# Kernel optimization log

Measured on AMD Instinct MI355X. Metric: run time of the kernel, lower is better.

## Reference

```python
import jax, jax.numpy as jnp
import numpy as np

N = 2048      # spatial nodes
K = 4         # blanket size (timesteps)
C = 128       # channels
H = 4         # heads
D = C // H    # head dim
MOD = 256     # mod_features
CTX = 7       # context_features (3+4)
B = 1
TN = N * K


def _make_edges():
    """Faithful numpy port of create_spatio_temporal_edges."""
    rng = np.random.default_rng(0)
    loops = np.stack([np.arange(N), np.arange(N)], axis=1)
    rnd = rng.integers(0, N, size=(N * 15, 2))
    self_edges = np.concatenate([loops, rnd])          # (32768, 2), every node has an edge
    cross_edges = rng.integers(0, N, size=(N * 8, 2))  # (16384, 2)
    spatial = (np.arange(K)[:, None, None] * N + self_edges[None]).reshape(-1, 2)
    temporal = (np.arange(K)[:, None, None] * N + cross_edges[None]).reshape(-1, 2)
    tq, tk = temporal[:, 0], temporal[:, 1]
    E = cross_edges.shape[0]
    parts = [spatial] + [np.stack([tq, np.roll(tk, -(k + 1) * E)], axis=-1) for k in range(K - 1)]
    return np.concatenate(parts).astype(np.int32)   # (327680, 2)


def setup_inputs() -> dict:
    key = jax.random.key(0)
    ks = jax.random.split(key, 16)
    def g(i, shape, scale=0.02):
        return jax.random.normal(ks[i], shape, dtype=jnp.float32) * scale
    return {
        "x": jax.random.normal(ks[0], (B, TN, C), dtype=jnp.float32),
        "time_encoding": jax.random.normal(ks[1], (B, MOD), dtype=jnp.float32),
        "context_encoding": jax.random.normal(ks[2], (B, K, N, CTX), dtype=jnp.float32),
        "edge_index": jnp.asarray(_make_edges()),
        "mod_w1": g(3, (MOD, MOD)), "mod_b1": jnp.zeros((MOD,), jnp.float32),
        "mod_w2": g(4, (3 * C, MOD), 0.0002), "mod_b2": jnp.zeros((3 * C,), jnp.float32),  # last linear scaled by 0.01
        "siren_w0": g(5, (C, CTX), 0.5), "siren_b0": jnp.zeros((C,), jnp.float32),
        "siren_w1": g(6, (C, C)), "siren_b1": jnp.zeros((C,), jnp.float32),
        "wq": g(7, (C, C)), "bq": jnp.zeros((C,), jnp.float32),
        "wk": g(8, (C, C)), "bk": jnp.zeros((C,), jnp.float32),
        "wv": g(9, (C, C)), "bv": jnp.zeros((C,), jnp.float32),
        "wo": g(10, (C, C)), "bo": jnp.zeros((C,), jnp.float32),
        "ffn_w1": g(11, (4 * C, C)), "ffn_b1": jnp.zeros((4 * C,), jnp.float32),
        "ffn_w2": g(12, (C, 4 * C)), "ffn_b2": jnp.zeros((C,), jnp.float32),
    }


def _ln(z, eps=1e-5):
    m = jnp.mean(z, axis=-1, keepdims=True)
    v = jnp.var(z, axis=-1, keepdims=True)
    return (z - m) * jax.lax.rsqrt(v + eps)


def reference(x, time_encoding, context_encoding, edge_index,
              mod_w1, mod_b1, mod_w2, mod_b2,
              siren_w0, siren_b0, siren_w1, siren_b1,
              wq, bq, wk, bk, wv, bv, wo, bo,
              ffn_w1, ffn_b1, ffn_w2, ffn_b2):
    Bx, TNx, Cx = x.shape
    Dh = Cx // H
    # AdaLN modulation: Linear -> SiLU -> Linear -> split into (a, b, c), each (B,1,C)
    t = jax.nn.silu(time_encoding @ mod_w1.T + mod_b1)
    mod = (t @ mod_w2.T + mod_b2).reshape(Bx, 3, Cx)
    a, b, c = mod[:, 0][:, None, :], mod[:, 1][:, None, :], mod[:, 2][:, None, :]
    # SIREN context embedding (1 sin layer + output linear)
    hctx = jnp.sin(context_encoding @ siren_w0.T + siren_b0)
    ctx = (hctx @ siren_w1.T + siren_b1).reshape(Bx, TNx, Cx)
    y = (a + 1.0) * _ln(x + ctx) + b
    # Graph attention over edge list (qk_norm = per-head LayerNorm, no affine)
    q = _ln((y @ wq.T + bq).reshape(Bx, TNx, H, Dh))
    k = _ln((y @ wk.T + bk).reshape(Bx, TNx, H, Dh))
    v = (y @ wv.T + bv).reshape(Bx, TNx, H, Dh)
    src, dst = edge_index[:, 0], edge_index[:, 1]  # query node, key node
    qT = jnp.transpose(q, (1, 0, 2, 3))  # (TN,B,H,D): segment axis first
    kT = jnp.transpose(k, (1, 0, 2, 3))
    vT = jnp.transpose(v, (1, 0, 2, 3))
    qe, ke, ve = qT[src], kT[dst], vT[dst]             # (E,B,H,D)
    s = jnp.einsum('ebhd,ebhd->ebh', qe, ke) / jnp.sqrt(jnp.float32(Dh))
    m = jax.ops.segment_max(s, src, num_segments=TNx)  # (TN,B,H)
    p = jnp.exp(s - m[src])
    denom = jax.ops.segment_sum(p, src, num_segments=TNx)
    agg = jax.ops.segment_sum(p[..., None] * ve, src, num_segments=TNx)  # (TN,B,H,D)
    attn = agg / jnp.maximum(denom, 1e-9)[..., None]
    attn = jnp.transpose(attn, (1, 0, 2, 3)).reshape(Bx, TNx, Cx) @ wo.T + bo
    y = y + attn
    # FFN (no inner residual, matches original)
    y = jax.nn.silu(y @ ffn_w1.T + ffn_b1) @ ffn_w2.T + ffn_b2
    # rsqrt-scaled residual combine
    return (x + c * y) * jax.lax.rsqrt(1.0 + c * c)
```

## Files before the change

kernel.cpp:

```cpp
#include <hip/hip_runtime.h>
#include <math.h>

#define TNODES 8192
#define CC 128
#define RT 32
#define DEGCAP 128

typedef __attribute__((ext_vector_type(8))) short bf8;
typedef __attribute__((ext_vector_type(4))) float fx4;

__device__ __forceinline__ ushort f2b(float f){
  union { float f; uint u; } a; a.f = f;
  uint u = a.u;
  uint r = (u + 0x7fffu + ((u >> 16) & 1u)) >> 16;
  return (ushort)r;
}
__device__ __forceinline__ float b2f(ushort s){
  union { uint u; float f; } a; a.u = ((uint)s) << 16;
  return a.f;
}
__device__ __forceinline__ float2 bpair(uint u){
  union { uint u; float f; } lo, hi;
  lo.u = u << 16; hi.u = u & 0xffff0000u;
  float2 r; r.x = lo.f; r.y = hi.f; return r;
}
#define SWZ(row, col) ((col) ^ (((row) & 7) << 3))

__global__ __launch_bounds__(256) void s1_setup(
    const float* __restrict__ sw1, const float* __restrict__ wq, const float* __restrict__ wk,
    const float* __restrict__ wv, const float* __restrict__ wo, const float* __restrict__ fw1,
    const float* __restrict__ fw2, ushort* __restrict__ dst,
    int* __restrict__ cnt,
    const float* __restrict__ te, const float* __restrict__ mw1, const float* __restrict__ mb1,
    float* __restrict__ tbuf)
{
  const int b = blockIdx.x, tid = threadIdx.x;
  if (b < 208){
    int i = (b * 256 + tid) * 4;
    const float* src; int off;
    if      (i <  16384){ src = sw1; off = i; }
    else if (i <  32768){ src = wq;  off = i - 16384; }
    else if (i <  49152){ src = wk;  off = i - 32768; }
    else if (i <  65536){ src = wv;  off = i - 49152; }
    else if (i <  81920){ src = wo;  off = i - 65536; }
    else if (i < 147456){ src = fw1; off = i - 81920; }
    else                { src = fw2; off = i - 147456; }
    float4 v = *(const float4*)&src[off];
    ushort4 o; o.x = f2b(v.x); o.y = f2b(v.y); o.z = f2b(v.z); o.w = f2b(v.w);
    *(ushort4*)&dst[i] = o;
  } else if (b < 240){
    cnt[(b - 208) * 256 + tid] = 0;
  } else {
    const int og = tid >> 4, th = tid & 15;
    const int o = (b - 240) * 16 + og;
    float acc = 0.f;
    #pragma unroll
    for (int u = 0; u < 4; ++u){
      float4 w  = *(const float4*)&mw1[o*256 + th*16 + u*4];
      float4 t4 = *(const float4*)&te[th*16 + u*4];
      acc += w.x*t4.x + w.y*t4.y + w.z*t4.z + w.w*t4.w;
    }
    #pragma unroll
    for (int m = 1; m < 16; m <<= 1) acc += __shfl_xor(acc, m);
    if (th == 0){
      float z = acc + mb1[o];
      tbuf[o] = z / (1.f + __expf(-z));
    }
  }
}

__global__ __launch_bounds__(512) void k2_ctx_y_qkv(
    const float* __restrict__ x, const float* __restrict__ ce,
    const float* __restrict__ sw0, const float* __restrict__ sb0,
    const ushort* __restrict__ sw1b, const float* __restrict__ sb1,
    const ushort* __restrict__ wqb, const float* __restrict__ bq,
    const ushort* __restrict__ wkb, const float* __restrict__ bk,
    const ushort* __restrict__ wvb, const float* __restrict__ bv,
    const float* __restrict__ tbuf, const float* __restrict__ mw2, const float* __restrict__ mb2,
    ushort* __restrict__ Ybf, ushort* __restrict__ Qb, ushort* __restrict__ Kb, ushort* __restrict__ Vb,
    const int* __restrict__ ei, int E, int* __restrict__ cnt, int* __restrict__ adj)
{
  __shared__ float  ceL[RT][8];
  __shared__ float  tbL[256];
  __shared__ float  modL[256];
  __shared__ ushort hxb[RT*CC];
  __shared__ float  yL[RT][132];
  __shared__ ushort yb[RT*CC];
  const int tid  = threadIdx.x;

  if (blockIdx.x >= TNODES/RT){
    const int b = blockIdx.x - TNODES/RT;
    int e0 = (b * 512 + tid) * 2;
    if (e0 + 1 < E){
      int4 p = *(const int4*)&ei[2*e0];
      int s;
      s = atomicAdd(&cnt[p.x], 1); adj[p.x*DEGCAP + (s & (DEGCAP-1))] = p.y;
      s = atomicAdd(&cnt[p.z], 1); adj[p.z*DEGCAP + (s & (DEGCAP-1))] = p.w;
    } else if (e0 < E){
      int sr = ei[2*e0], ds = ei[2*e0+1];
      int s = atomicAdd(&cnt[sr], 1);
      adj[sr*DEGCAP + (s & (DEGCAP-1))] = ds;
    }
    return;
  }

  const int lane = tid & 63, wave = tid >> 6;
  const int l15 = lane & 15, lg = lane >> 4;
  const int hw  = wave & 3;
  const int rtb = (wave >> 2) * 16;
  const int row0 = blockIdx.x * RT;

  if (tid < RT*7){ int r = tid/7, i = tid - r*7; ceL[r][i] = ce[(row0+r)*7 + i]; }
  if (tid < 256) tbL[tid] = tbuf[tid];
  __syncthreads();

  #pragma unroll
  for (int u = 0; u < 8; ++u){
    int idx = tid + u*512;
    int r = idx >> 7, j = idx & 127;
    float a = sb0[j];
    #pragma unroll
    for (int i = 0; i < 7; ++i) a += sw0[j*7+i]*ceL[r][i];
    hxb[r*CC + SWZ(r, j)] = f2b(__sinf(a));
  }

  {
    const int g = tid >> 4, th = tid & 15;
    #pragma unroll
    for (int it = 0; it < 8; ++it){
      int o = g*8 + it;
      float acc = 0.f;
      #pragma unroll
      for (int u = 0; u < 4; ++u){
        float4 wv = *(const float4*)&mw2[o*256 + th*16 + u*4];
        float4 t4 = *(const float4*)&tbL[th*16 + u*4];
        acc += wv.x*t4.x + wv.y*t4.y + wv.z*t4.z + wv.w*t4.w;
      }
      #pragma unroll
      for (int m = 1; m < 16; m <<= 1) acc += __shfl_xor(acc, m);
      if (th == 0) modL[o] = acc + mb2[o];
    }
  }
  __syncthreads();

  const int colb = hw*32;
  {
    bf8 aH[4], bB[8];
    #pragma unroll
    for (int ks = 0; ks < 4; ++ks)
      aH[ks] = *(const bf8*)&hxb[(rtb+l15)*CC + SWZ(rtb+l15, ks*32 + lg*8)];
    #pragma unroll
    for (int ks = 0; ks < 4; ++ks)
      #pragma unroll
      for (int n = 0; n < 2; ++n)
        bB[ks*2+n] = *(const bf8*)&sw1b[(colb + n*16 + l15)*CC + ks*32 + lg*8];
    fx4 acc[2]; acc[0] = 0.f; acc[1] = 0.f;
    #pragma unroll
    for (int ks = 0; ks < 4; ++ks){
      acc[0] = __builtin_amdgcn_mfma_f32_16x16x32_bf16(aH[ks], bB[ks*2+0], acc[0], 0, 0, 0);
      acc[1] = __builtin_amdgcn_mfma_f32_16x16x32_bf16(aH[ks], bB[ks*2+1], acc[1], 0, 0, 0);
    }
    #pragma unroll
    for (int n = 0; n < 2; ++n)
      #pragma unroll
      for (int q = 0; q < 4; ++q){
        int r = rtb + lg*4 + q, c = colb + n*16 + l15;
        yL[r][c] = x[(row0+r)*CC + c] + acc[n][q] + sb1[c];
      }
  }
  __syncthreads();

  {
    int r = tid >> 4, s16 = tid & 15;
    float4 za = *(const float4*)&yL[r][s16*8];
    float4 zb = *(const float4*)&yL[r][s16*8 + 4];
    float sum = za.x+za.y+za.z+za.w + zb.x+zb.y+zb.z+zb.w;
    float ssq = za.x*za.x+za.y*za.y+za.z*za.z+za.w*za.w
              + zb.x*zb.x+zb.y*zb.y+zb.z*zb.z+zb.w*zb.w;
    #pragma unroll
    for (int m = 1; m < 16; m <<= 1){ sum += __shfl_xor(sum, m); ssq += __shfl_xor(ssq, m); }
    float mean = sum * (1.f/128.f);
    float var  = ssq * (1.f/128.f) - mean*mean;
    float inv  = rsqrtf(var + 1e-5f);
    float zv[8] = {za.x,za.y,za.z,za.w,zb.x,zb.y,zb.z,zb.w};
    bf8 pk;
    #pragma unroll
    for (int u = 0; u < 8; ++u){
      int jj = s16*8 + u;
      float z = (zv[u] - mean) * inv;
      pk[u] = (short)f2b((1.f + modL[jj]) * z + modL[128+jj]);
    }
    *(bf8*)&yb[r*CC + SWZ(r, s16*8)] = pk;
  }
  __syncthreads();

  {
    int rr = tid >> 4, b8 = tid & 15;
    bf8 v = *(const bf8*)&yb[rr*CC + SWZ(rr, b8*8)];
    *(bf8*)&Ybf[(row0+rr)*CC + b8*8] = v;
  }

  bf8 af[4];
  #pragma unroll
  for (int ks = 0; ks < 4; ++ks)
    af[ks] = *(const bf8*)&yb[(rtb+l15)*CC + SWZ(rtb+l15, ks*32 + lg*8)];

  const ushort* Wb[3] = {wqb, wkb, wvb};
  const float*  Bs[3] = {bq, bk, bv};
  ushort*       Ob[3] = {Qb, Kb, Vb};
  const int cb = hw*32;
  #pragma unroll
  for (int m = 0; m < 3; ++m){
    bf8 bB[8];
    #pragma unroll
    for (int ks = 0; ks < 4; ++ks)
      #pragma unroll
      for (int n = 0; n < 2; ++n)
        bB[ks*2+n] = *(const bf8*)&Wb[m][(cb + n*16 + l15)*CC + ks*32 + lg*8];
    fx4 acc[2]; acc[0] = 0.f; acc[1] = 0.f;
    #pragma unroll
    for (int ks = 0; ks < 4; ++ks){
      acc[0] = __builtin_amdgcn_mfma_f32_16x16x32_bf16(af[ks], bB[ks*2+0], acc[0], 0, 0, 0);
      acc[1] = __builtin_amdgcn_mfma_f32_16x16x32_bf16(af[ks], bB[ks*2+1], acc[1], 0, 0, 0);
    }
    float vals[2][4];
    #pragma unroll
    for (int n = 0; n < 2; ++n)
      #pragma unroll
      for (int q = 0; q < 4; ++q)
        vals[n][q] = acc[n][q] + Bs[m][cb + n*16 + l15];
    if (m < 2){
      #pragma unroll
      for (int q = 0; q < 4; ++q){
        float s  = vals[0][q] + vals[1][q];
        float ss = vals[0][q]*vals[0][q] + vals[1][q]*vals[1][q];
        #pragma unroll
        for (int mm = 1; mm < 16; mm <<= 1){ s += __shfl_xor(s, mm); ss += __shfl_xor(ss, mm); }
        float mean = s * (1.f/32.f);
        float var  = ss * (1.f/32.f) - mean*mean;
        float inv  = rsqrtf(var + 1e-5f);
        vals[0][q] = (vals[0][q] - mean) * inv;
        vals[1][q] = (vals[1][q] - mean) * inv;
      }
    }
    #pragma unroll
    for (int n = 0; n < 2; ++n)
      #pragma unroll
      for (int q = 0; q < 4; ++q){
        int r = rtb + lg*4 + q, c = cb + n*16 + l15;
        Ob[m][(row0+r)*CC + c] = f2b(vals[n][q]);
      }
  }
}

__global__ __launch_bounds__(512) void k45_attn_ffn(
    const float* __restrict__ x, const ushort* __restrict__ Ybf,
    const ushort* __restrict__ Qb, const ushort* __restrict__ Kb, const ushort* __restrict__ Vb,
    const int* __restrict__ cnt, const int* __restrict__ adj,
    const ushort* __restrict__ wob, const float* __restrict__ bo,
    const ushort* __restrict__ fw1b, const float* __restrict__ fb1,
    const ushort* __restrict__ fw2b, const float* __restrict__ fb2,
    const float* __restrict__ tbuf, const float* __restrict__ mw2, const float* __restrict__ mb2,
    float* __restrict__ out)
{
  __shared__ float  tbL[256];
  __shared__ float  cL[128];
  __shared__ ushort aLb[RT*CC];
  __shared__ ushort yyb[RT*CC];
  __shared__ ushort h1b[RT*512];
  const int tid  = threadIdx.x;
  const int lane = tid & 63, w = tid >> 6;
  const int l15 = lane & 15, lg = lane >> 4;
  const int row0 = blockIdx.x * RT;

  if (tid < 256) tbL[tid] = tbuf[tid];
  __syncthreads();

  {
    const int g = tid >> 4, th = tid & 15;
    #pragma unroll
    for (int it = 0; it < 4; ++it){
      int o = g*4 + it;
      float acc = 0.f;
      #pragma unroll
      for (int u = 0; u < 4; ++u){
        float4 wv = *(const float4*)&mw2[(256+o)*256 + th*16 + u*4];
        float4 t4 = *(const float4*)&tbL[th*16 + u*4];
        acc += wv.x*t4.x + wv.y*t4.y + wv.z*t4.z + wv.w*t4.w;
      }
      #pragma unroll
      for (int m = 1; m < 16; m <<= 1) acc += __shfl_xor(acc, m);
      if (th == 0) cL[o] = acc + mb2[256+o];
    }
  }

  {
    const int quarter = lane >> 4, ql = lane & 15;
    const int src = row0 + w*4 + quarter;

    uint4 qr = *(const uint4*)&Qb[src*CC + 8*ql];
    float2 qa = bpair(qr.x), qb = bpair(qr.y), qc = bpair(qr.z), qd = bpair(qr.w);
    const float sc = 0.17677669529663687f;
    qa.x*=sc; qa.y*=sc; qb.x*=sc; qb.y*=sc; qc.x*=sc; qc.y*=sc; qd.x*=sc; qd.y*=sc;

    float a0=0.f,a1=0.f,a2=0.f,a3=0.f,a4=0.f,a5=0.f,a6=0.f,a7=0.f, dh=0.f;
    const int deg = min(cnt[src], DEGCAP);
    const int* ab = adj + src*DEGCAP;
    int dmax = deg;
    dmax = max(dmax, __shfl_xor(dmax, 16));
    dmax = max(dmax, __shfl_xor(dmax, 32));

    for (int e = 0; e < dmax; e += 4){
      int4 dd = *(const int4*)&ab[e];
      int d0 = (e   < deg) ? dd.x : 0;
      int d1 = (e+1 < deg) ? dd.y : 0;
      int d2 = (e+2 < deg) ? dd.z : 0;
      int d3 = (e+3 < deg) ? dd.w : 0;
      uint4 k0 = *(const uint4*)&Kb[d0*CC + 8*ql];
      uint4 k1 = *(const uint4*)&Kb[d1*CC + 8*ql];
      uint4 k2 = *(const uint4*)&Kb[d2*CC + 8*ql];
      uint4 k3 = *(const uint4*)&Kb[d3*CC + 8*ql];
      uint4 v0 = *(const uint4*)&Vb[d0*CC + 8*ql];
      uint4 v1 = *(const uint4*)&Vb[d1*CC + 8*ql];
      uint4 v2 = *(const uint4*)&Vb[d2*CC + 8*ql];
      uint4 v3 = *(const uint4*)&Vb[d3*CC + 8*ql];
      float2 x0, x1, x2, x3;
      x0 = bpair(k0.x); x1 = bpair(k0.y); x2 = bpair(k0.z); x3 = bpair(k0.w);
      float p0 = qa.x*x0.x+qa.y*x0.y + qb.x*x1.x+qb.y*x1.y + qc.x*x2.x+qc.y*x2.y + qd.x*x3.x+qd.y*x3.y;
      x0 = bpair(k1.x); x1 = bpair(k1.y); x2 = bpair(k1.z); x3 = bpair(k1.w);
      float p1 = qa.x*x0.x+qa.y*x0.y + qb.x*x1.x+qb.y*x1.y + qc.x*x2.x+qc.y*x2.y + qd.x*x3.x+qd.y*x3.y;
      x0 = bpair(k2.x); x1 = bpair(k2.y); x2 = bpair(k2.z); x3 = bpair(k2.w);
      float p2 = qa.x*x0.x+qa.y*x0.y + qb.x*x1.x+qb.y*x1.y + qc.x*x2.x+qc.y*x2.y + qd.x*x3.x+qd.y*x3.y;
      x0 = bpair(k3.x); x1 = bpair(k3.y); x2 = bpair(k3.z); x3 = bpair(k3.w);
      float p3 = qa.x*x0.x+qa.y*x0.y + qb.x*x1.x+qb.y*x1.y + qc.x*x2.x+qc.y*x2.y + qd.x*x3.x+qd.y*x3.y;
      p0 += __shfl_xor(p0, 1); p1 += __shfl_xor(p1, 1); p2 += __shfl_xor(p2, 1); p3 += __shfl_xor(p3, 1);
      p0 += __shfl_xor(p0, 2); p1 += __shfl_xor(p1, 2); p2 += __shfl_xor(p2, 2); p3 += __shfl_xor(p3, 2);
      p0 = (e   < deg) ? __expf(p0) : 0.f;
      p1 = (e+1 < deg) ? __expf(p1) : 0.f;
      p2 = (e+2 < deg) ? __expf(p2) : 0.f;
      p3 = (e+3 < deg) ? __expf(p3) : 0.f;
      x0 = bpair(v0.x); x1 = bpair(v0.y); x2 = bpair(v0.z); x3 = bpair(v0.w);
      a0 += p0*x0.x; a1 += p0*x0.y; a2 += p0*x1.x; a3 += p0*x1.y;
      a4 += p0*x2.x; a5 += p0*x2.y; a6 += p0*x3.x; a7 += p0*x3.y;
      x0 = bpair(v1.x); x1 = bpair(v1.y); x2 = bpair(v1.z); x3 = bpair(v1.w);
      a0 += p1*x0.x; a1 += p1*x0.y; a2 += p1*x1.x; a3 += p1*x1.y;
      a4 += p1*x2.x; a5 += p1*x2.y; a6 += p1*x3.x; a7 += p1*x3.y;
      x0 = bpair(v2.x); x1 = bpair(v2.y); x2 = bpair(v2.z); x3 = bpair(v2.w);
      a0 += p2*x0.x; a1 += p2*x0.y; a2 += p2*x1.x; a3 += p2*x1.y;
      a4 += p2*x2.x; a5 += p2*x2.y; a6 += p2*x3.x; a7 += p2*x3.y;
      x0 = bpair(v3.x); x1 = bpair(v3.y); x2 = bpair(v3.z); x3 = bpair(v3.w);
      a0 += p3*x0.x; a1 += p3*x0.y; a2 += p3*x1.x; a3 += p3*x1.y;
      a4 += p3*x2.x; a5 += p3*x2.y; a6 += p3*x3.x; a7 += p3*x3.y;
      dh += p0 + p1 + p2 + p3;
    }
    float invd = 1.f / fmaxf(dh, 1e-9f);
    uint4 o4;
    o4.x = (uint)f2b(a0*invd) | ((uint)f2b(a1*invd) << 16);
    o4.y = (uint)f2b(a2*invd) | ((uint)f2b(a3*invd) << 16);
    o4.z = (uint)f2b(a4*invd) | ((uint)f2b(a5*invd) << 16);
    o4.w = (uint)f2b(a6*invd) | ((uint)f2b(a7*invd) << 16);
    int r = w*4 + quarter;
    *(uint4*)&aLb[r*CC + SWZ(r, 8*ql)] = o4;
  }
  __syncthreads();

  {
    const int cw = w*16;
    bf8 aA[2][4], bB[4];
    #pragma unroll
    for (int rt = 0; rt < 2; ++rt)
      #pragma unroll
      for (int ks = 0; ks < 4; ++ks)
        aA[rt][ks] = *(const bf8*)&aLb[(rt*16+l15)*CC + SWZ(rt*16+l15, ks*32 + lg*8)];
    #pragma unroll
    for (int ks = 0; ks < 4; ++ks)
      bB[ks] = *(const bf8*)&wob[(cw + l15)*CC + ks*32 + lg*8];
    fx4 acc[2]; acc[0] = 0.f; acc[1] = 0.f;
    #pragma unroll
    for (int ks = 0; ks < 4; ++ks){
      acc[0] = __builtin_amdgcn_mfma_f32_16x16x32_bf16(aA[0][ks], bB[ks], acc[0], 0, 0, 0);
      acc[1] = __builtin_amdgcn_mfma_f32_16x16x32_bf16(aA[1][ks], bB[ks], acc[1], 0, 0, 0);
    }
    #pragma unroll
    for (int rt = 0; rt < 2; ++rt)
      #pragma unroll
      for (int q = 0; q < 4; ++q){
        int r = rt*16 + lg*4 + q, c = cw + l15;
        float yy = b2f(Ybf[(row0+r)*CC + c]) + acc[rt][q] + bo[c];
        yyb[r*CC + SWZ(r, c)] = f2b(yy);
      }
  }
  __syncthreads();

  {
    const int cb1 = w*64;
    bf8 aY[2][4];
    #pragma unroll
    for (int rt = 0; rt < 2; ++rt)
      #pragma unroll
      for (int ks = 0; ks < 4; ++ks)
        aY[rt][ks] = *(const bf8*)&yyb[(rt*16+l15)*CC + SWZ(rt*16+l15, ks*32 + lg*8)];
    fx4 h[2][4];
    #pragma unroll
    for (int rt = 0; rt < 2; ++rt)
      #pragma unroll
      for (int n = 0; n < 4; ++n) h[rt][n] = 0.f;
    #pragma unroll
    for (int kp = 0; kp < 2; ++kp){
      bf8 bB[8];
      #pragma unroll
      for (int kk = 0; kk < 2; ++kk)
        #pragma unroll
        for (int n = 0; n < 4; ++n)
          bB[kk*4+n] = *(const bf8*)&fw1b[(cb1 + n*16 + l15)*CC + (kp*2+kk)*32 + lg*8];
      #pragma unroll
      for (int kk = 0; kk < 2; ++kk)
        #pragma unroll
        for (int n = 0; n < 4; ++n){
          h[0][n] = __builtin_amdgcn_mfma_f32_16x16x32_bf16(aY[0][kp*2+kk], bB[kk*4+n], h[0][n], 0, 0, 0);
          h[1][n] = __builtin_amdgcn_mfma_f32_16x16x32_bf16(aY[1][kp*2+kk], bB[kk*4+n], h[1][n], 0, 0, 0);
        }
    }
    #pragma unroll
    for (int rt = 0; rt < 2; ++rt)
      #pragma unroll
      for (int n = 0; n < 4; ++n)
        #pragma unroll
        for (int q = 0; q < 4; ++q){
          int r = rt*16 + lg*4 + q, c = cb1 + n*16 + l15;
          float z = h[rt][n][q] + fb1[c];
          float sl = z / (1.f + __expf(-z));
          h1b[r*512 + SWZ(r, c)] = f2b(sl);
        }
  }
  __syncthreads();

  {
    const int cw = w*16;
    fx4 acc[2]; acc[0] = 0.f; acc[1] = 0.f;
    #pragma unroll
    for (int g4 = 0; g4 < 4; ++g4){
      bf8 aH[2][4], bB[4];
      #pragma unroll
      for (int rt = 0; rt < 2; ++rt)
        #pragma unroll
        for (int kk = 0; kk < 4; ++kk)
          aH[rt][kk] = *(const bf8*)&h1b[(rt*16+l15)*512 + SWZ(rt*16+l15, (g4*4+kk)*32 + lg*8)];
      #pragma unroll
      for (int kk = 0; kk < 4; ++kk)
        bB[kk] = *(const bf8*)&fw2b[(cw + l15)*512 + (g4*4+kk)*32 + lg*8];
      #pragma unroll
      for (int kk = 0; kk < 4; ++kk){
        acc[0] = __builtin_amdgcn_mfma_f32_16x16x32_bf16(aH[0][kk], bB[kk], acc[0], 0, 0, 0);
        acc[1] = __builtin_amdgcn_mfma_f32_16x16x32_bf16(aH[1][kk], bB[kk], acc[1], 0, 0, 0);
      }
    }
    #pragma unroll
    for (int rt = 0; rt < 2; ++rt)
      #pragma unroll
      for (int q = 0; q < 4; ++q){
        int r = rt*16 + lg*4 + q, c = cw + l15;
        int g = row0 + r;
        float cj = cL[c];
        float y2 = acc[rt][q] + fb2[c];
        out[g*CC + c] = (x[g*CC + c] + cj*y2) * rsqrtf(1.f + cj*cj);
      }
  }
}

extern "C" void kernel_launch(void* const* d_in, const int* in_sizes, int n_in,
                              void* d_out, int out_size, void* d_ws, size_t ws_size,
                              hipStream_t stream)
{
  const float* x   = (const float*)d_in[0];
  const float* te  = (const float*)d_in[1];
  const float* ce  = (const float*)d_in[2];
  const int*   ei  = (const int*)  d_in[3];
  const float* mw1 = (const float*)d_in[4];
  const float* mb1 = (const float*)d_in[5];
  const float* mw2 = (const float*)d_in[6];
  const float* mb2 = (const float*)d_in[7];
  const float* sw0 = (const float*)d_in[8];
  const float* sb0 = (const float*)d_in[9];
  const float* sw1 = (const float*)d_in[10];
  const float* sb1 = (const float*)d_in[11];
  const float* wq  = (const float*)d_in[12];
  const float* bq  = (const float*)d_in[13];
  const float* wk  = (const float*)d_in[14];
  const float* bk  = (const float*)d_in[15];
  const float* wv  = (const float*)d_in[16];
  const float* bv  = (const float*)d_in[17];
  const float* wo  = (const float*)d_in[18];
  const float* bo  = (const float*)d_in[19];
  const float* fw1 = (const float*)d_in[20];
  const float* fb1 = (const float*)d_in[21];
  const float* fw2 = (const float*)d_in[22];
  const float* fb2 = (const float*)d_in[23];
  float* out = (float*)d_out;
  const int E = in_sizes[3] / 2;

  float* ws   = (float*)d_ws;
  float* tbuf = ws;
  ushort* WB  = (ushort*)(ws + 1024);
  ushort* sw1b = WB;
  ushort* wqb  = WB + 16384;
  ushort* wkb  = WB + 32768;
  ushort* wvb  = WB + 49152;
  ushort* wob  = WB + 65536;
  ushort* fw1b = WB + 81920;
  ushort* fw2b = WB + 147456;
  ushort* Ybf = WB + 212992;
  ushort* Qb  = Ybf + TNODES*CC;
  ushort* Kb  = Qb  + TNODES*CC;
  ushort* Vb  = Kb  + TNODES*CC;
  int* cnt    = (int*)(Vb + TNODES*CC);
  int* adj    = cnt + TNODES;

  const int nSB = (E + 1023) / 1024;

  s1_setup<<<256, 256, 0, stream>>>(sw1, wq, wk, wv, wo, fw1, fw2, WB, cnt, te, mw1, mb1, tbuf);
  k2_ctx_y_qkv<<<TNODES/RT + nSB, 512, 0, stream>>>(x, ce, sw0, sb0, sw1b, sb1,
                                              wqb, bq, wkb, bk, wvb, bv,
                                              tbuf, mw2, mb2, Ybf, Qb, Kb, Vb,
                                              ei, E, cnt, adj);
  k45_attn_ffn<<<TNODES/RT, 512, 0, stream>>>(x, Ybf, Qb, Kb, Vb, cnt, adj,
                                              wob, bo, fw1b, fb1, fw2b, fb2,
                                              tbuf, mw2, mb2, out);
}
```

Measured before the change: 73.42 us.

## Halve attention/FFN row tile, spread each node over 32 lanes, prefetch gathers

The fused attention+FFN kernel now handles 16 rows per block instead of 32, doubling the grid, and asks for 4 blocks per CU through launch bounds. In the edge-gather loop each source node is served by 32 lanes loading 4 bf16 values each instead of 16 lanes loading 8, so fewer rows sit idle waiting on the slowest neighbour. The K/V gathers for the next group of 4 edges are software-prefetched into registers. The aim is more latency hiding for the irregular gather, at the cost of an extra shuffle step, more register pressure and re-reading the weights from twice as many blocks in the MFMA stages.

```diff
diff --git a/kernel.cpp b/kernel.cpp
--- a/kernel.cpp
+++ b/kernel.cpp
@@ -3,7 +3,8 @@
 
 #define TNODES 8192
 #define CC 128
-#define RT 32
+#define RT2 32
+#define RT5 16
 #define DEGCAP 128
 
 typedef __attribute__((ext_vector_type(8))) short bf8;
@@ -80,16 +81,16 @@
     ushort* __restrict__ Ybf, ushort* __restrict__ Qb, ushort* __restrict__ Kb, ushort* __restrict__ Vb,
     const int* __restrict__ ei, int E, int* __restrict__ cnt, int* __restrict__ adj)
 {
-  __shared__ float  ceL[RT][8];
+  __shared__ float  ceL[RT2][8];
   __shared__ float  tbL[256];
   __shared__ float  modL[256];
-  __shared__ ushort hxb[RT*CC];
-  __shared__ float  yL[RT][132];
-  __shared__ ushort yb[RT*CC];
+  __shared__ ushort hxb[RT2*CC];
+  __shared__ float  yL[RT2][132];
+  __shared__ ushort yb[RT2*CC];
   const int tid  = threadIdx.x;
 
-  if (blockIdx.x >= TNODES/RT){
-    const int b = blockIdx.x - TNODES/RT;
+  if (blockIdx.x >= TNODES/RT2){
+    const int b = blockIdx.x - TNODES/RT2;
     int e0 = (b * 512 + tid) * 2;
     if (e0 + 1 < E){
       int4 p = *(const int4*)&ei[2*e0];
@@ -108,9 +109,9 @@
   const int l15 = lane & 15, lg = lane >> 4;
   const int hw  = wave & 3;
   const int rtb = (wave >> 2) * 16;
-  const int row0 = blockIdx.x * RT;
-
-  if (tid < RT*7){ int r = tid/7, i = tid - r*7; ceL[r][i] = ce[(row0+r)*7 + i]; }
+  const int row0 = blockIdx.x * RT2;
+
+  if (tid < RT2*7){ int r = tid/7, i = tid - r*7; ceL[r][i] = ce[(row0+r)*7 + i]; }
   if (tid < 256) tbL[tid] = tbuf[tid];
   __syncthreads();
 
@@ -253,7 +254,7 @@
   }
 }
 
-__global__ __launch_bounds__(512) void k45_attn_ffn(
+__global__ __launch_bounds__(512, 4) void k45_attn_ffn(
     const float* __restrict__ x, const ushort* __restrict__ Ybf,
     const ushort* __restrict__ Qb, const ushort* __restrict__ Kb, const ushort* __restrict__ Vb,
     const int* __restrict__ cnt, const int* __restrict__ adj,
@@ -265,13 +266,13 @@
 {
   __shared__ float  tbL[256];
   __shared__ float  cL[128];
-  __shared__ ushort aLb[RT*CC];
-  __shared__ ushort yyb[RT*CC];
-  __shared__ ushort h1b[RT*512];
+  __shared__ ushort aLb[RT5*CC];
+  __shared__ ushort yyb[RT5*CC];
+  __shared__ ushort h1b[RT5*512];
   const int tid  = threadIdx.x;
   const int lane = tid & 63, w = tid >> 6;
   const int l15 = lane & 15, lg = lane >> 4;
-  const int row0 = blockIdx.x * RT;
+  const int row0 = blockIdx.x * RT5;
 
   if (tid < 256) tbL[tid] = tbuf[tid];
   __syncthreads();
@@ -295,116 +296,122 @@
   }
 
   {
-    const int quarter = lane >> 4, ql = lane & 15;
-    const int src = row0 + w*4 + quarter;
-
-    uint4 qr = *(const uint4*)&Qb[src*CC + 8*ql];
-    float2 qa = bpair(qr.x), qb = bpair(qr.y), qc = bpair(qr.z), qd = bpair(qr.w);
+    const int half = lane >> 5, hl = lane & 31;
+    const int src = row0 + w*2 + half;
+
+    uint2 qraw = *(const uint2*)&Qb[src*CC + 4*hl];
+    float2 q0 = bpair(qraw.x), q1 = bpair(qraw.y);
     const float sc = 0.17677669529663687f;
-    qa.x*=sc; qa.y*=sc; qb.x*=sc; qb.y*=sc; qc.x*=sc; qc.y*=sc; qd.x*=sc; qd.y*=sc;
-
-    float a0=0.f,a1=0.f,a2=0.f,a3=0.f,a4=0.f,a5=0.f,a6=0.f,a7=0.f, dh=0.f;
+    q0.x*=sc; q0.y*=sc; q1.x*=sc; q1.y*=sc;
+
+    float a0=0.f, a1=0.f, a2=0.f, a3=0.f, dh=0.f;
     const int deg = min(cnt[src], DEGCAP);
     const int* ab = adj + src*DEGCAP;
-    int dmax = deg;
-    dmax = max(dmax, __shfl_xor(dmax, 16));
-    dmax = max(dmax, __shfl_xor(dmax, 32));
-
-    for (int e = 0; e < dmax; e += 4){
-      int4 dd = *(const int4*)&ab[e];
-      int d0 = (e   < deg) ? dd.x : 0;
-      int d1 = (e+1 < deg) ? dd.y : 0;
-      int d2 = (e+2 < deg) ? dd.z : 0;
-      int d3 = (e+3 < deg) ? dd.w : 0;
-      uint4 k0 = *(const uint4*)&Kb[d0*CC + 8*ql];
-      uint4 k1 = *(const uint4*)&Kb[d1*CC + 8*ql];
-      uint4 k2 = *(const uint4*)&Kb[d2*CC + 8*ql];
-      uint4 k3 = *(const uint4*)&Kb[d3*CC + 8*ql];
-      uint4 v0 = *(const uint4*)&Vb[d0*CC + 8*ql];
-      uint4 v1 = *(const uint4*)&Vb[d1*CC + 8*ql];
-      uint4 v2 = *(const uint4*)&Vb[d2*CC + 8*ql];
-      uint4 v3 = *(const uint4*)&Vb[d3*CC + 8*ql];
-      float2 x0, x1, x2, x3;
-      x0 = bpair(k0.x); x1 = bpair(k0.y); x2 = bpair(k0.z); x3 = bpair(k0.w);
-      float p0 = qa.x*x0.x+qa.y*x0.y + qb.x*x1.x+qb.y*x1.y + qc.x*x2.x+qc.y*x2.y + qd.x*x3.x+qd.y*x3.y;
-      x0 = bpair(k1.x); x1 = bpair(k1.y); x2 = bpair(k1.z); x3 = bpair(k1.w);
-      float p1 = qa.x*x0.x+qa.y*x0.y + qb.x*x1.x+qb.y*x1.y + qc.x*x2.x+qc.y*x2.y + qd.x*x3.x+qd.y*x3.y;
-      x0 = bpair(k2.x); x1 = bpair(k2.y); x2 = bpair(k2.z); x3 = bpair(k2.w);
-      float p2 = qa.x*x0.x+qa.y*x0.y + qb.x*x1.x+qb.y*x1.y + qc.x*x2.x+qc.y*x2.y + qd.x*x3.x+qd.y*x3.y;
-      x0 = bpair(k3.x); x1 = bpair(k3.y); x2 = bpair(k3.z); x3 = bpair(k3.w);
-      float p3 = qa.x*x0.x+qa.y*x0.y + qb.x*x1.x+qb.y*x1.y + qc.x*x2.x+qc.y*x2.y + qd.x*x3.x+qd.y*x3.y;
+    int dmax = max(deg, __shfl_xor(deg, 32));
+    const int niter = (dmax + 3) >> 2;
+
+    uint2 k0,k1,k2,k3,v0,v1,v2,v3;
+    {
+      int4 dd = *(const int4*)&ab[0];
+      int d0 = dd.x;
+      int d1 = (1 < deg) ? dd.y : 0;
+      int d2 = (2 < deg) ? dd.z : 0;
+      int d3 = (3 < deg) ? dd.w : 0;
+      k0 = *(const uint2*)&Kb[d0*CC + 4*hl];
+      k1 = *(const uint2*)&Kb[d1*CC + 4*hl];
+      k2 = *(const uint2*)&Kb[d2*CC + 4*hl];
+      k3 = *(const uint2*)&Kb[d3*CC + 4*hl];
+      v0 = *(const uint2*)&Vb[d0*CC + 4*hl];
+      v1 = *(const uint2*)&Vb[d1*CC + 4*hl];
+      v2 = *(const uint2*)&Vb[d2*CC + 4*hl];
+      v3 = *(const uint2*)&Vb[d3*CC + 4*hl];
+    }
+
+    for (int i = 0; i < niter; ++i){
+      const int e = i*4;
+      uint2 ck0=k0, ck1=k1, ck2=k2, ck3=k3, cv0=v0, cv1=v1, cv2=v2, cv3=v3;
+      if (i + 1 < niter){
+        int en = e + 4;
+        int4 dd = *(const int4*)&ab[en];
+        int d0 = (en   < deg) ? dd.x : 0;
+        int d1 = (en+1 < deg) ? dd.y : 0;
+        int d2 = (en+2 < deg) ? dd.z : 0;
+        int d3 = (en+3 < deg) ? dd.w : 0;
+        k0 = *(const uint2*)&Kb[d0*CC + 4*hl];
+        k1 = *(const uint2*)&Kb[d1*CC + 4*hl];
+        k2 = *(const uint2*)&Kb[d2*CC + 4*hl];
+        k3 = *(const uint2*)&Kb[d3*CC + 4*hl];
+        v0 = *(const uint2*)&Vb[d0*CC + 4*hl];
+        v1 = *(const uint2*)&Vb[d1*CC + 4*hl];
+        v2 = *(const uint2*)&Vb[d2*CC + 4*hl];
+        v3 = *(const uint2*)&Vb[d3*CC + 4*hl];
+      }
+      float2 f0, f1;
+      f0 = bpair(ck0.x); f1 = bpair(ck0.y);
+      float p0 = q0.x*f0.x + q0.y*f0.y + q1.x*f1.x + q1.y*f1.y;
+      f0 = bpair(ck1.x); f1 = bpair(ck1.y);
+      float p1 = q0.x*f0.x + q0.y*f0.y + q1.x*f1.x + q1.y*f1.y;
+      f0 = bpair(ck2.x); f1 = bpair(ck2.y);
+      float p2 = q0.x*f0.x + q0.y*f0.y + q1.x*f1.x + q1.y*f1.y;
+      f0 = bpair(ck3.x); f1 = bpair(ck3.y);
+      float p3 = q0.x*f0.x + q0.y*f0.y + q1.x*f1.x + q1.y*f1.y;
       p0 += __shfl_xor(p0, 1); p1 += __shfl_xor(p1, 1); p2 += __shfl_xor(p2, 1); p3 += __shfl_xor(p3, 1);
       p0 += __shfl_xor(p0, 2); p1 += __shfl_xor(p1, 2); p2 += __shfl_xor(p2, 2); p3 += __shfl_xor(p3, 2);
+      p0 += __shfl_xor(p0, 4); p1 += __shfl_xor(p1, 4); p2 += __shfl_xor(p2, 4); p3 += __shfl_xor(p3, 4);
       p0 = (e   < deg) ? __expf(p0) : 0.f;
       p1 = (e+1 < deg) ? __expf(p1) : 0.f;
       p2 = (e+2 < deg) ? __expf(p2) : 0.f;
       p3 = (e+3 < deg) ? __expf(p3) : 0.f;
-      x0 = bpair(v0.x); x1 = bpair(v0.y); x2 = bpair(v0.z); x3 = bpair(v0.w);
-      a0 += p0*x0.x; a1 += p0*x0.y; a2 += p0*x1.x; a3 += p0*x1.y;
-      a4 += p0*x2.x; a5 += p0*x2.y; a6 += p0*x3.x; a7 += p0*x3.y;
-      x0 = bpair(v1.x); x1 = bpair(v1.y); x2 = bpair(v1.z); x3 = bpair(v1.w);
-      a0 += p1*x0.x; a1 += p1*x0.y; a2 += p1*x1.x; a3 += p1*x1.y;
-      a4 += p1*x2.x; a5 += p1*x2.y; a6 += p1*x3.x; a7 += p1*x3.y;
-      x0 = bpair(v2.x); x1 = bpair(v2.y); x2 = bpair(v2.z); x3 = bpair(v2.w);
-      a0 += p2*x0.x; a1 += p2*x0.y; a2 += p2*x1.x; a3 += p2*x1.y;
-      a4 += p2*x2.x; a5 += p2*x2.y; a6 += p2*x3.x; a7 += p2*x3.y;
-      x0 = bpair(v3.x); x1 = bpair(v3.y); x2 = bpair(v3.z); x3 = bpair(v3.w);
-      a0 += p3*x0.x; a1 += p3*x0.y; a2 += p3*x1.x; a3 += p3*x1.y;
-      a4 += p3*x2.x; a5 += p3*x2.y; a6 += p3*x3.x; a7 += p3*x3.y;
+      f0 = bpair(cv0.x); f1 = bpair(cv0.y);
+      a0 += p0*f0.x; a1 += p0*f0.y; a2 += p0*f1.x; a3 += p0*f1.y;
+      f0 = bpair(cv1.x); f1 = bpair(cv1.y);
+      a0 += p1*f0.x; a1 += p1*f0.y; a2 += p1*f1.x; a3 += p1*f1.y;
+      f0 = bpair(cv2.x); f1 = bpair(cv2.y);
+      a0 += p2*f0.x; a1 += p2*f0.y; a2 += p2*f1.x; a3 += p2*f1.y;
+      f0 = bpair(cv3.x); f1 = bpair(cv3.y);
+      a0 += p3*f0.x; a1 += p3*f0.y; a2 += p3*f1.x; a3 += p3*f1.y;
       dh += p0 + p1 + p2 + p3;
     }
     float invd = 1.f / fmaxf(dh, 1e-9f);
-    uint4 o4;
-    o4.x = (uint)f2b(a0*invd) | ((uint)f2b(a1*invd) << 16);
-    o4.y = (uint)f2b(a2*invd) | ((uint)f2b(a3*invd) << 16);
-    o4.z = (uint)f2b(a4*invd) | ((uint)f2b(a5*invd) << 16);
-    o4.w = (uint)f2b(a6*invd) | ((uint)f2b(a7*invd) << 16);
-    int r = w*4 + quarter;
-    *(uint4*)&aLb[r*CC + SWZ(r, 8*ql)] = o4;
+    uint2 o2;
+    o2.x = (uint)f2b(a0*invd) | ((uint)f2b(a1*invd) << 16);
+    o2.y = (uint)f2b(a2*invd) | ((uint)f2b(a3*invd) << 16);
+    int r = w*2 + half;
+    *(uint2*)&aLb[r*CC + SWZ(r, 4*hl)] = o2;
   }
   __syncthreads();
 
   {
     const int cw = w*16;
-    bf8 aA[2][4], bB[4];
-    #pragma unroll
-    for (int rt = 0; rt < 2; ++rt)
-      #pragma unroll
-      for (int ks = 0; ks < 4; ++ks)
-        aA[rt][ks] = *(const bf8*)&aLb[(rt*16+l15)*CC + SWZ(rt*16+l15, ks*32 + lg*8)];
+    bf8 aA[4], bB[4];
+    #pragma unroll
+    for (int ks = 0; ks < 4; ++ks)
+      aA[ks] = *(const bf8*)&aLb[l15*CC + SWZ(l15, ks*32 + lg*8)];
     #pragma unroll
     for (int ks = 0; ks < 4; ++ks)
       bB[ks] = *(const bf8*)&wob[(cw + l15)*CC + ks*32 + lg*8];
-    fx4 acc[2]; acc[0] = 0.f; acc[1] = 0.f;
-    #pragma unroll
-    for (int ks = 0; ks < 4; ++ks){
-      acc[0] = __builtin_amdgcn_mfma_f32_16x16x32_bf16(aA[0][ks], bB[ks], acc[0], 0, 0, 0);
-      acc[1] = __builtin_amdgcn_mfma_f32_16x16x32_bf16(aA[1][ks], bB[ks], acc[1], 0, 0, 0);
-    }
-    #pragma unroll
-    for (int rt = 0; rt < 2; ++rt)
-      #pragma unroll
-      for (int q = 0; q < 4; ++q){
-        int r = rt*16 + lg*4 + q, c = cw + l15;
-        float yy = b2f(Ybf[(row0+r)*CC + c]) + acc[rt][q] + bo[c];
-        yyb[r*CC + SWZ(r, c)] = f2b(yy);
-      }
+    fx4 acc; acc = 0.f;
+    #pragma unroll
+    for (int ks = 0; ks < 4; ++ks)
+      acc = __builtin_amdgcn_mfma_f32_16x16x32_bf16(aA[ks], bB[ks], acc, 0, 0, 0);
+    #pragma unroll
+    for (int q = 0; q < 4; ++q){
+      int r = lg*4 + q, c = cw + l15;
+      float yy = b2f(Ybf[(row0+r)*CC + c]) + acc[q] + bo[c];
+      yyb[r*CC + SWZ(r, c)] = f2b(yy);
+    }
   }
   __syncthreads();
 
   {
     const int cb1 = w*64;
-    bf8 aY[2][4];
-    #pragma unroll
-    for (int rt = 0; rt < 2; ++rt)
-      #pragma unroll
-      for (int ks = 0; ks < 4; ++ks)
-        aY[rt][ks] = *(const bf8*)&yyb[(rt*16+l15)*CC + SWZ(rt*16+l15, ks*32 + lg*8)];
-    fx4 h[2][4];
-    #pragma unroll
-    for (int rt = 0; rt < 2; ++rt)
-      #pragma unroll
-      for (int n = 0; n < 4; ++n) h[rt][n] = 0.f;
+    bf8 aY[4];
+    #pragma unroll
+    for (int ks = 0; ks < 4; ++ks)
+      aY[ks] = *(const bf8*)&yyb[l15*CC + SWZ(l15, ks*32 + lg*8)];
+    fx4 h[4];
+    #pragma unroll
+    for (int n = 0; n < 4; ++n) h[n] = 0.f;
     #pragma unroll
     for (int kp = 0; kp < 2; ++kp){
       bf8 bB[8];
@@ -416,55 +423,45 @@
       #pragma unroll
       for (int kk = 0; kk < 2; ++kk)
         #pragma unroll
-        for (int n = 0; n < 4; ++n){
-          h[0][n] = __builtin_amdgcn_mfma_f32_16x16x32_bf16(aY[0][kp*2+kk], bB[kk*4+n], h[0][n], 0, 0, 0);
-          h[1][n] = __builtin_amdgcn_mfma_f32_16x16x32_bf16(aY[1][kp*2+kk], bB[kk*4+n], h[1][n], 0, 0, 0);
-        }
-    }
-    #pragma unroll
-    for (int rt = 0; rt < 2; ++rt)
-      #pragma unroll
-      for (int n = 0; n < 4; ++n)
-        #pragma unroll
-        for (int q = 0; q < 4; ++q){
-          int r = rt*16 + lg*4 + q, c = cb1 + n*16 + l15;
-          float z = h[rt][n][q] + fb1[c];
-          float sl = z / (1.f + __expf(-z));
-          h1b[r*512 + SWZ(r, c)] = f2b(sl);
-        }
+        for (int n = 0; n < 4; ++n)
+          h[n] = __builtin_amdgcn_mfma_f32_16x16x32_bf16(aY[kp*2+kk], bB[kk*4+n], h[n], 0, 0, 0);
+    }
+    #pragma unroll
+    for (int n = 0; n < 4; ++n)
+      #pragma unroll
+      for (int q = 0; q < 4; ++q){
+        int r = lg*4 + q, c = cb1 + n*16 + l15;
+        float z = h[n][q] + fb1[c];
+        float sl = z / (1.f + __expf(-z));
+        h1b[r*512 + SWZ(r, c)] = f2b(sl);
+      }
   }
   __syncthreads();
 
   {
     const int cw = w*16;
-    fx4 acc[2]; acc[0] = 0.f; acc[1] = 0.f;
+    fx4 acc; acc = 0.f;
     #pragma unroll
     for (int g4 = 0; g4 < 4; ++g4){
-      bf8 aH[2][4], bB[4];
-      #pragma unroll
-      for (int rt = 0; rt < 2; ++rt)
-        #pragma unroll
-        for (int kk = 0; kk < 4; ++kk)
-          aH[rt][kk] = *(const bf8*)&h1b[(rt*16+l15)*512 + SWZ(rt*16+l15, (g4*4+kk)*32 + lg*8)];
+      bf8 aH[4], bB[4];
+      #pragma unroll
+      for (int kk = 0; kk < 4; ++kk)
+        aH[kk] = *(const bf8*)&h1b[l15*512 + SWZ(l15, (g4*4+kk)*32 + lg*8)];
       #pragma unroll
       for (int kk = 0; kk < 4; ++kk)
         bB[kk] = *(const bf8*)&fw2b[(cw + l15)*512 + (g4*4+kk)*32 + lg*8];
       #pragma unroll
-      for (int kk = 0; kk < 4; ++kk){
-        acc[0] = __builtin_amdgcn_mfma_f32_16x16x32_bf16(aH[0][kk], bB[kk], acc[0], 0, 0, 0);
-        acc[1] = __builtin_amdgcn_mfma_f32_16x16x32_bf16(aH[1][kk], bB[kk], acc[1], 0, 0, 0);
-      }
-    }
-    #pragma unroll
-    for (int rt = 0; rt < 2; ++rt)
-      #pragma unroll
-      for (int q = 0; q < 4; ++q){
-        int r = rt*16 + lg*4 + q, c = cw + l15;
-        int g = row0 + r;
-        float cj = cL[c];
-        float y2 = acc[rt][q] + fb2[c];
-        out[g*CC + c] = (x[g*CC + c] + cj*y2) * rsqrtf(1.f + cj*cj);
-      }
+      for (int kk = 0; kk < 4; ++kk)
+        acc = __builtin_amdgcn_mfma_f32_16x16x32_bf16(aH[kk], bB[kk], acc, 0, 0, 0);
+    }
+    #pragma unroll
+    for (int q = 0; q < 4; ++q){
+      int r = lg*4 + q, c = cw + l15;
+      int g = row0 + r;
+      float cj = cL[c];
+      float y2 = acc[q] + fb2[c];
+      out[g*CC + c] = (x[g*CC + c] + cj*y2) * rsqrtf(1.f + cj*cj);
+    }
   }
 }
 
@@ -519,11 +516,11 @@
   const int nSB = (E + 1023) / 1024;
 
   s1_setup<<<256, 256, 0, stream>>>(sw1, wq, wk, wv, wo, fw1, fw2, WB, cnt, te, mw1, mb1, tbuf);
-  k2_ctx_y_qkv<<<TNODES/RT + nSB, 512, 0, stream>>>(x, ce, sw0, sb0, sw1b, sb1,
+  k2_ctx_y_qkv<<<TNODES/RT2 + nSB, 512, 0, stream>>>(x, ce, sw0, sb0, sw1b, sb1,
                                               wqb, bq, wkb, bk, wvb, bv,
                                               tbuf, mw2, mb2, Ybf, Qb, Kb, Vb,
                                               ei, E, cnt, adj);
-  k45_attn_ffn<<<TNODES/RT, 512, 0, stream>>>(x, Ybf, Qb, Kb, Vb, cnt, adj,
-                                              wob, bo, fw1b, fb1, fw2b, fb2,
-                                              tbuf, mw2, mb2, out);
-}
+  k45_attn_ffn<<<TNODES/RT5, 512, 0, stream>>>(x, Ybf, Qb, Kb, Vb, cnt, adj,
+                                               wob, bo, fw1b, fb1, fw2b, fb2,
+                                               tbuf, mw2, mb2, out);
+}
```

Measured after the change: 81.44 us. 1.11x slower.
